# Optimization experiments

Hardware: AMD Instinct MI355X
Metric: run time of the kernel (lower is better)

Reference implementation:

```python
import jax, jax.numpy as jnp
import numpy as np

NEG_SLOPE = 0.2
EPS = 1e-16
N_NODES = 50000
N_EDGES = 800000
D_IN = 128
D_E = 64
HEADS = 4
D_OUT = 32


def setup_inputs() -> dict:
    key = jax.random.key(0)
    k1, k2, k3, k4, k5, k6 = jax.random.split(key, 6)
    H = jax.random.normal(k1, (N_NODES, D_IN), dtype=jnp.float32)
    edge_index = jax.random.randint(k2, (2, N_EDGES), 0, N_NODES, dtype=jnp.int64)
    E = jax.random.normal(k3, (N_EDGES, D_E), dtype=jnp.float32)
    # torch nn.Linear weights: [out_features, in_features]
    W = jax.random.normal(k4, (HEADS * D_OUT, D_IN), dtype=jnp.float32) * (1.0 / np.sqrt(D_IN))
    W_e = jax.random.normal(k5, (HEADS * D_OUT, D_E), dtype=jnp.float32) * (1.0 / np.sqrt(D_E))
    att = jax.random.normal(k6, (1, HEADS, D_OUT), dtype=jnp.float32) * 0.1
    return {"H": H, "edge_index": edge_index, "E": E, "W": W, "W_e": W_e, "att": att}


def reference(H, edge_index, E, W, W_e, att):
    n_nodes = H.shape[0]
    # node transform: [N, heads, d_out]
    HT = (H @ W.T).reshape(n_nodes, HEADS, D_OUT)
    src, dst = edge_index[0], edge_index[1]
    # edge transform: [E, heads, d_out]
    ET = (E @ W_e.T).reshape(-1, HEADS, D_OUT)
    alpha_in = HT[src] + HT[dst] + ET              # [E, heads, d_out]
    alpha_in = jax.nn.leaky_relu(alpha_in, NEG_SLOPE)
    alpha = jnp.sum(alpha_in * att, axis=-1)        # [E, heads]
    # segment softmax over incoming edges of each dst node
    a_max = jax.ops.segment_max(alpha, dst, num_segments=n_nodes)   # [N, heads]
    alpha = jnp.exp(alpha - a_max[dst])
    a_sum = jax.ops.segment_sum(alpha, dst, num_segments=n_nodes)   # [N, heads]
    alpha = alpha / (a_sum[dst] + EPS)
    # weighted aggregation of source features
    messages = HT[src] * alpha[:, :, None]          # [E, heads, d_out]
    H_out = jax.ops.segment_sum(messages, dst, num_segments=n_nodes)  # [N, heads, d_out]
    return H_out.reshape(n_nodes, HEADS * D_OUT)    # concat=True
```

## Files before the change

kernel.cpp:

```cpp
#include <hip/hip_runtime.h>

#define N_NODES 50000
#define N_EDGES 800000
#define D_IN    128
#define D_E     64
#define NH      4
#define F_TOT   128
#define NEG_SLOPE 0.2f

typedef __attribute__((ext_vector_type(8))) short short8;
typedef __attribute__((ext_vector_type(4))) float f32x4;

__device__ __forceinline__ short f2bf(float x) {
    unsigned u = __float_as_uint(x);
    u += 0x7FFFu + ((u >> 16) & 1u);
    return (short)(u >> 16);
}

__global__ __launch_bounds__(256) void k_node_transform(
    const float* __restrict__ H, const float* __restrict__ W,
    float* __restrict__ HT)
{
    __shared__ float wt[D_IN * F_TOT];
    const int tid = threadIdx.x;
    for (int i = tid; i < D_IN * F_TOT; i += 256) {
        const int f = i & 127, k = i >> 7;
        wt[k * F_TOT + f] = W[f * D_IN + k];
    }
    __syncthreads();

    const int l = tid & 63;
    const int w = tid >> 6;
    const int gwave  = blockIdx.x * 4 + w;
    const int nwaves = gridDim.x * 4;
    const int ngroups = N_NODES / 8;

    for (int grp = gwave; grp < ngroups; grp += nwaves) {
        const int g = grp * 8;
        float ax[8], ay[8];
#pragma unroll
        for (int j = 0; j < 8; ++j) { ax[j] = 0.f; ay[j] = 0.f; }

        for (int k4 = 0; k4 < D_IN / 4; ++k4) {
            float hv[8][4];
#pragma unroll
            for (int j = 0; j < 8; ++j)
                *(float4*)hv[j] = *(const float4*)&H[(size_t)(g + j) * D_IN + k4 * 4];
#pragma unroll
            for (int kk = 0; kk < 4; ++kk) {
                const float2 wk = *(const float2*)&wt[(k4 * 4 + kk) * F_TOT + 2 * l];
#pragma unroll
                for (int j = 0; j < 8; ++j) {
                    ax[j] = fmaf(wk.x, hv[j][kk], ax[j]);
                    ay[j] = fmaf(wk.y, hv[j][kk], ay[j]);
                }
            }
        }
#pragma unroll
        for (int j = 0; j < 8; ++j) {
            float2 r; r.x = ax[j]; r.y = ay[j];
            *(float2*)&HT[(size_t)(g + j) * F_TOT + 2 * l] = r;
        }
    }
}

__global__ __launch_bounds__(256) void k_hist(
    const int* __restrict__ EI, int* __restrict__ deg)
{
    const int e = blockIdx.x * 256 + threadIdx.x;
    if (e < N_EDGES) atomicAdd(&deg[EI[N_EDGES + e]], 1);
}

__global__ __launch_bounds__(1024) void k_scan(
    const int* __restrict__ deg, int* __restrict__ row_start,
    int* __restrict__ cursor)
{
    __shared__ int wsum[16];
    __shared__ int carry;
    const int tid = threadIdx.x;
    const int l = tid & 63;
    const int wv = tid >> 6;
    if (tid == 0) carry = 0;

    for (int base = 0; base < N_NODES; base += 1024) {
        __syncthreads();
        const int cb = carry;
        const int i = base + tid;
        const int v = (i < N_NODES) ? deg[i] : 0;
        int x = v;
#pragma unroll
        for (int off = 1; off < 64; off <<= 1) {
            int t = __shfl_up(x, off, 64);
            if (l >= off) x += t;
        }
        if (l == 63) wsum[wv] = x;
        __syncthreads();
        int wave_off = 0;
        for (int k = 0; k < wv; ++k) wave_off += wsum[k];
        int tot = 0;
#pragma unroll
        for (int k = 0; k < 16; ++k) tot += wsum[k];
        const int excl = cb + wave_off + (x - v);
        if (i < N_NODES) { row_start[i] = excl; cursor[i] = excl; }
        __syncthreads();
        if (tid == 0) carry = cb + tot;
    }
    __syncthreads();
    if (tid == 0) row_start[N_NODES] = carry;
}

__global__ __launch_bounds__(256, 3) void k_logits(
    const float* __restrict__ E, const int* __restrict__ EI,
    const float* __restrict__ We, const float* __restrict__ att,
    const float* __restrict__ HT,
    float* __restrict__ wperm, int* __restrict__ srcperm,
    int* __restrict__ cursor)
{
    __shared__ short8 s_bf[8][2][64];
    __shared__ f32x4  s_att[8][4];

    const int tid = threadIdx.x;
    const int l   = tid & 63;
    const int wv  = tid >> 6;
    const int r16 = l & 15;
    const int g4  = l >> 4;

    if (wv == 0) {
#pragma unroll
        for (int ft = 0; ft < 8; ++ft) {
#pragma unroll
            for (int kc = 0; kc < 2; ++kc) {
                const float* wp = &We[(size_t)(ft * 16 + r16) * D_E + kc * 32 + g4 * 8];
                const f32x4 lo = *(const f32x4*)wp;
                const f32x4 hi = *(const f32x4*)(wp + 4);
                short8 b;
                b[0] = f2bf(lo[0]); b[1] = f2bf(lo[1]); b[2] = f2bf(lo[2]); b[3] = f2bf(lo[3]);
                b[4] = f2bf(hi[0]); b[5] = f2bf(hi[1]); b[6] = f2bf(hi[2]); b[7] = f2bf(hi[3]);
                s_bf[ft][kc][l] = b;
            }
        }
        if (l < 32) {
            const int ft = l >> 2, g = l & 3;
            s_att[ft][g] = *(const f32x4*)&att[ft * 16 + g * 4];
        }
    }
    __syncthreads();

    const int gwave  = blockIdx.x * 4 + wv;
    const int nwaves = gridDim.x * 4;
    const int ntiles = N_EDGES / 16;

    for (int t = gwave; t < ntiles; t += nwaves) {
        const int e0 = t * 16;
        const int e  = e0 + r16;
        const int sr = EI[e];
        const int dr = EI[N_EDGES + e];

        int pos = 0;
        if (l < 16) pos = atomicAdd(&cursor[dr], 1);

        const float* hsp = &HT[(size_t)sr * F_TOT + g4 * 4];
        const float* hdp = &HT[(size_t)dr * F_TOT + g4 * 4];
        f32x4 hs4[8], hd4[8];
#pragma unroll
        for (int ft = 0; ft < 8; ++ft) {
            hs4[ft] = *(const f32x4*)(hsp + ft * 16);
            hd4[ft] = *(const f32x4*)(hdp + ft * 16);
        }

        short8 af[2];
#pragma unroll
        for (int kc = 0; kc < 2; ++kc) {
            const float* ep = &E[(size_t)e * D_E + kc * 32 + g4 * 8];
            const f32x4 lo = *(const f32x4*)ep;
            const f32x4 hi = *(const f32x4*)(ep + 4);
            short8 a;
            a[0] = f2bf(lo[0]); a[1] = f2bf(lo[1]); a[2] = f2bf(lo[2]); a[3] = f2bf(lo[3]);
            a[4] = f2bf(hi[0]); a[5] = f2bf(hi[1]); a[6] = f2bf(hi[2]); a[7] = f2bf(hi[3]);
            af[kc] = a;
        }

        float ph[4] = {0.f, 0.f, 0.f, 0.f};
#pragma unroll
        for (int ft = 0; ft < 8; ++ft) {
            f32x4 z = {0.f, 0.f, 0.f, 0.f};
            z = __builtin_amdgcn_mfma_f32_16x16x32_bf16(s_bf[ft][0][l], af[0], z, 0, 0, 0);
            const f32x4 acc =
                __builtin_amdgcn_mfma_f32_16x16x32_bf16(s_bf[ft][1][l], af[1], z, 0, 0, 0);
            const f32x4 at = s_att[ft][g4];
#pragma unroll
            for (int r = 0; r < 4; ++r) {
                float v = hs4[ft][r] + hd4[ft][r] + acc[r];
                v = v > 0.f ? v : NEG_SLOPE * v;
                ph[ft >> 1] = fmaf(v, at[r], ph[ft >> 1]);
            }
        }
#pragma unroll
        for (int h = 0; h < 4; ++h) {
            ph[h] += __shfl_xor(ph[h], 16, 64);
            ph[h] += __shfl_xor(ph[h], 32, 64);
        }
        if (l < 16) {
            f32x4 w;
            w[0] = __expf(ph[0]); w[1] = __expf(ph[1]);
            w[2] = __expf(ph[2]); w[3] = __expf(ph[3]);
            *(f32x4*)&wperm[(size_t)4 * pos] = w;
            srcperm[pos] = sr;
        }
    }
}

__global__ __launch_bounds__(256, 8) void k_aggregate(
    const float* __restrict__ HT, const float* __restrict__ wperm,
    const int* __restrict__ srcperm, const int* __restrict__ row_start,
    float* __restrict__ out)
{
    const int tid = threadIdx.x;
    const int l = tid & 63;
    const int wv = tid >> 6;
    const int n = blockIdx.x * 4 + wv;
    if (n >= N_NODES) return;
    const int h = l >> 4;
    const int beg = row_start[n];
    const int end = row_start[n + 1];

    float ax = 0.f, ay = 0.f, sw = 0.f;
    for (int base = beg; base < end; base += 16) {
        const int   svl = (l < 16 && base + l < end) ? srcperm[base + l] : 0;
        const float wvl = (4 * base + l < 4 * end) ? wperm[4 * base + l] : 0.f;
#pragma unroll
        for (int j = 0; j < 16; ++j) {
            const int   s = __shfl(svl, j, 64);
            const float w = __shfl(wvl, 4 * j + h, 64);
            const float2 hs = *(const float2*)&HT[(size_t)s * F_TOT + 2 * l];
            ax = fmaf(w, hs.x, ax);
            ay = fmaf(w, hs.y, ay);
            sw += w;
        }
    }
    const float inv = 1.f / (sw + 1e-16f);
    float2 r; r.x = ax * inv; r.y = ay * inv;
    *(float2*)&out[(size_t)n * F_TOT + 2 * l] = r;
}

extern "C" void kernel_launch(void* const* d_in, const int* in_sizes, int n_in,
                              void* d_out, int out_size, void* d_ws, size_t ws_size,
                              hipStream_t stream)
{
    const float* H   = (const float*)d_in[0];
    const int*   EI  = (const int*)d_in[1];
    const float* E   = (const float*)d_in[2];
    const float* W   = (const float*)d_in[3];
    const float* We  = (const float*)d_in[4];
    const float* att = (const float*)d_in[5];
    float* out = (float*)d_out;

    float* HT        = (float*)d_ws;
    float* wperm     = HT + (size_t)N_NODES * F_TOT;
    int*   srcperm   = (int*)(wperm + (size_t)N_EDGES * NH);
    int*   deg       = srcperm + N_EDGES;
    int*   row_start = deg + N_NODES;
    int*   cursor    = row_start + N_NODES + 1;

    hipMemsetAsync(deg, 0, N_NODES * sizeof(int), stream);

    k_hist<<<(N_EDGES + 255) / 256, 256, 0, stream>>>(EI, deg);
    k_scan<<<1, 1024, 0, stream>>>(deg, row_start, cursor);
    k_node_transform<<<512, 256, 0, stream>>>(H, W, HT);
    k_logits<<<2048, 256, 0, stream>>>(E, EI, We, att, HT,
                                       wperm, srcperm, cursor);
    k_aggregate<<<(N_NODES + 3) / 4, 256, 0, stream>>>(HT, wperm, srcperm,
                                                       row_start, out);
}
```

Baseline: 669.0 us.

## Fuse edge logits with per-node aggregation via a dst-sorted edge permutation

```diff
diff --git a/kernel.cpp b/kernel.cpp
--- a/kernel.cpp
+++ b/kernel.cpp
@@ -109,12 +109,24 @@
     if (tid == 0) row_start[N_NODES] = carry;
 }
 
-__global__ __launch_bounds__(256, 3) void k_logits(
-    const float* __restrict__ E, const int* __restrict__ EI,
-    const float* __restrict__ We, const float* __restrict__ att,
-    const float* __restrict__ HT,
-    float* __restrict__ wperm, int* __restrict__ srcperm,
-    int* __restrict__ cursor)
+__global__ __launch_bounds__(256) void k_permute(
+    const int* __restrict__ EI, int* __restrict__ cursor,
+    int2* __restrict__ perm)
+{
+    const int e = blockIdx.x * 256 + threadIdx.x;
+    if (e < N_EDGES) {
+        const int src = EI[e];
+        const int dst = EI[N_EDGES + e];
+        const int pos = atomicAdd(&cursor[dst], 1);
+        perm[pos] = make_int2(e, src);
+    }
+}
+
+__global__ __launch_bounds__(256, 3) void k_fused(
+    const float* __restrict__ E, const float* __restrict__ We,
+    const float* __restrict__ att, const float* __restrict__ HT,
+    const int2* __restrict__ perm, const int* __restrict__ row_start,
+    float* __restrict__ out)
 {
     __shared__ short8 s_bf[8][2][64];
     __shared__ f32x4  s_att[8][4];
@@ -146,32 +158,38 @@
     }
     __syncthreads();
 
-    const int gwave  = blockIdx.x * 4 + wv;
-    const int nwaves = gridDim.x * 4;
-    const int ntiles = N_EDGES / 16;
-
-    for (int t = gwave; t < ntiles; t += nwaves) {
-        const int e0 = t * 16;
-        const int e  = e0 + r16;
-        const int sr = EI[e];
-        const int dr = EI[N_EDGES + e];
-
-        int pos = 0;
-        if (l < 16) pos = atomicAdd(&cursor[dr], 1);
+    const int n = blockIdx.x * 4 + wv;
+    if (n >= N_NODES) return;
+    const int beg = row_start[n];
+    const int end = row_start[n + 1];
+
+    f32x4 hd4[8];
+#pragma unroll
+    for (int ft = 0; ft < 8; ++ft)
+        hd4[ft] = *(const f32x4*)&HT[(size_t)n * F_TOT + ft * 16 + g4 * 4];
+
+    f32x4 am[8];
+#pragma unroll
+    for (int ft = 0; ft < 8; ++ft) am[ft] = (f32x4){0.f, 0.f, 0.f, 0.f};
+    float sw[4] = {0.f, 0.f, 0.f, 0.f};
+
+    for (int t = beg; t < end; t += 16) {
+        const int  idx   = t + r16;
+        const bool valid = idx < end;
+        const int2 pe    = perm[valid ? idx : end - 1];
+        const int  eid   = pe.x;
+        const int  sr    = pe.y;
 
         const float* hsp = &HT[(size_t)sr * F_TOT + g4 * 4];
-        const float* hdp = &HT[(size_t)dr * F_TOT + g4 * 4];
-        f32x4 hs4[8], hd4[8];
-#pragma unroll
-        for (int ft = 0; ft < 8; ++ft) {
+        f32x4 hs4[8];
+#pragma unroll
+        for (int ft = 0; ft < 8; ++ft)
             hs4[ft] = *(const f32x4*)(hsp + ft * 16);
-            hd4[ft] = *(const f32x4*)(hdp + ft * 16);
-        }
 
         short8 af[2];
 #pragma unroll
         for (int kc = 0; kc < 2; ++kc) {
-            const float* ep = &E[(size_t)e * D_E + kc * 32 + g4 * 8];
+            const float* ep = &E[(size_t)eid * D_E + kc * 32 + g4 * 8];
             const f32x4 lo = *(const f32x4*)ep;
             const f32x4 hi = *(const f32x4*)(ep + 4);
             short8 a;
@@ -200,47 +218,44 @@
             ph[h] += __shfl_xor(ph[h], 16, 64);
             ph[h] += __shfl_xor(ph[h], 32, 64);
         }
-        if (l < 16) {
-            f32x4 w;
-            w[0] = __expf(ph[0]); w[1] = __expf(ph[1]);
-            w[2] = __expf(ph[2]); w[3] = __expf(ph[3]);
-            *(f32x4*)&wperm[(size_t)4 * pos] = w;
-            srcperm[pos] = sr;
-        }
-    }
-}
-
-__global__ __launch_bounds__(256, 8) void k_aggregate(
-    const float* __restrict__ HT, const float* __restrict__ wperm,
-    const int* __restrict__ srcperm, const int* __restrict__ row_start,
-    float* __restrict__ out)
-{
-    const int tid = threadIdx.x;
-    const int l = tid & 63;
-    const int wv = tid >> 6;
-    const int n = blockIdx.x * 4 + wv;
-    if (n >= N_NODES) return;
-    const int h = l >> 4;
-    const int beg = row_start[n];
-    const int end = row_start[n + 1];
-
-    float ax = 0.f, ay = 0.f, sw = 0.f;
-    for (int base = beg; base < end; base += 16) {
-        const int   svl = (l < 16 && base + l < end) ? srcperm[base + l] : 0;
-        const float wvl = (4 * base + l < 4 * end) ? wperm[4 * base + l] : 0.f;
-#pragma unroll
-        for (int j = 0; j < 16; ++j) {
-            const int   s = __shfl(svl, j, 64);
-            const float w = __shfl(wvl, 4 * j + h, 64);
-            const float2 hs = *(const float2*)&HT[(size_t)s * F_TOT + 2 * l];
-            ax = fmaf(w, hs.x, ax);
-            ay = fmaf(w, hs.y, ay);
-            sw += w;
-        }
-    }
-    const float inv = 1.f / (sw + 1e-16f);
-    float2 r; r.x = ax * inv; r.y = ay * inv;
-    *(float2*)&out[(size_t)n * F_TOT + 2 * l] = r;
+        float w[4];
+#pragma unroll
+        for (int h = 0; h < 4; ++h) {
+            w[h] = valid ? __expf(ph[h]) : 0.f;
+            sw[h] += w[h];
+        }
+#pragma unroll
+        for (int ft = 0; ft < 8; ++ft) {
+            const float wh = w[ft >> 1];
+#pragma unroll
+            for (int r = 0; r < 4; ++r)
+                am[ft][r] = fmaf(wh, hs4[ft][r], am[ft][r]);
+        }
+    }
+
+#pragma unroll
+    for (int m = 1; m < 16; m <<= 1) {
+#pragma unroll
+        for (int h = 0; h < 4; ++h) sw[h] += __shfl_xor(sw[h], m, 64);
+#pragma unroll
+        for (int ft = 0; ft < 8; ++ft)
+#pragma unroll
+            for (int r = 0; r < 4; ++r)
+                am[ft][r] += __shfl_xor(am[ft][r], m, 64);
+    }
+    float inv[4];
+#pragma unroll
+    for (int h = 0; h < 4; ++h) inv[h] = 1.f / (sw[h] + 1e-16f);
+
+    if (r16 == 0) {
+#pragma unroll
+        for (int ft = 0; ft < 8; ++ft) {
+            f32x4 o;
+#pragma unroll
+            for (int r = 0; r < 4; ++r) o[r] = am[ft][r] * inv[ft >> 1];
+            *(f32x4*)&out[(size_t)n * F_TOT + ft * 16 + g4 * 4] = o;
+        }
+    }
 }
 
 extern "C" void kernel_launch(void* const* d_in, const int* in_sizes, int n_in,
@@ -256,9 +271,8 @@
     float* out = (float*)d_out;
 
     float* HT        = (float*)d_ws;
-    float* wperm     = HT + (size_t)N_NODES * F_TOT;
-    int*   srcperm   = (int*)(wperm + (size_t)N_EDGES * NH);
-    int*   deg       = srcperm + N_EDGES;
+    int2*  perm      = (int2*)(HT + (size_t)N_NODES * F_TOT);
+    int*   deg       = (int*)(perm + N_EDGES);
     int*   row_start = deg + N_NODES;
     int*   cursor    = row_start + N_NODES + 1;
 
@@ -267,8 +281,7 @@
     k_hist<<<(N_EDGES + 255) / 256, 256, 0, stream>>>(EI, deg);
     k_scan<<<1, 1024, 0, stream>>>(deg, row_start, cursor);
     k_node_transform<<<512, 256, 0, stream>>>(H, W, HT);
-    k_logits<<<2048, 256, 0, stream>>>(E, EI, We, att, HT,
-                                       wperm, srcperm, cursor);
-    k_aggregate<<<(N_NODES + 3) / 4, 256, 0, stream>>>(HT, wperm, srcperm,
-                                                       row_start, out);
-}
+    k_permute<<<(N_EDGES + 255) / 256, 256, 0, stream>>>(EI, cursor, perm);
+    k_fused<<<(N_NODES + 3) / 4, 256, 0, stream>>>(E, We, att, HT,
+                                                   perm, row_start, out);
+}
```

Result: slower. 990.4 us (+48.0%).
